# Kernel tuning notes

Measured on AMD Instinct MI355X. Metric: run time of the kernel, lower is better.

The kernel has to match this reference:

```python
import jax, jax.numpy as jnp
import numpy as np
import math

B, S, D, H = 16, 256, 1024, 16
DK = D // H
MAXLEN = 512


def _sinusoid_table(maxlen, dim):
    # rows for positions -maxlen .. maxlen-1  (2*maxlen rows)
    pos = jnp.arange(-maxlen, maxlen, dtype=jnp.float32)[:, None]
    i = jnp.arange(dim)
    angle = pos / jnp.power(10000.0, (2 * (i // 2)) / dim).astype(jnp.float32)
    return jnp.where(i % 2 == 0, jnp.sin(angle), jnp.cos(angle))


def setup_inputs() -> dict:
    key = jax.random.key(0)
    ks = jax.random.split(key, 13)
    std_qk = math.sqrt(2.0 / (D + DK))
    inp = {
        "x": jax.random.normal(ks[0], (B, S, D), jnp.float32),
        "Wq": jax.random.normal(ks[1], (D, D), jnp.float32) * std_qk,
        "bq": jnp.zeros((D,), jnp.float32),
        "Wk": jax.random.normal(ks[2], (D, D), jnp.float32) * std_qk,
        "bk": jnp.zeros((D,), jnp.float32),
        "Wv": jax.random.normal(ks[3], (D, D), jnp.float32) * std_qk,
        "bv": jnp.zeros((D,), jnp.float32),
        "Wr": jax.random.normal(ks[4], (D, D), jnp.float32) * std_qk,
        "br": jnp.zeros((D,), jnp.float32),
        "u_bias": jax.random.normal(ks[5], (H, DK), jnp.float32) * math.sqrt(2.0 / (H + DK)),
        "v_bias": jax.random.normal(ks[6], (H, DK), jnp.float32) * math.sqrt(2.0 / (H + DK)),
        "Wo": jax.random.normal(ks[7], (D, D), jnp.float32) * math.sqrt(2.0 / (D + D)),
        "bo": jnp.zeros((D,), jnp.float32),
    }
    return inp


def reference(x, Wq, bq, Wk, bk, Wv, bv, Wr, br, u_bias, v_bias, Wo, bo):
    table = _sinusoid_table(MAXLEN, D)  # (2*MAXLEN, D)
    # relative position indices: idx[s, z] = z - s, shifted by +MAXLEN
    relpos_idx = (jnp.arange(2 * S)[None, :] - jnp.arange(S)[:, None])[:, :S] + MAXLEN
    relpos_vec = table[relpos_idx]  # (S, S, D)

    q = (x @ Wq.T + bq).reshape(B, S, H, DK)
    k = (x @ Wk.T + bk).reshape(B, S, H, DK)
    v = (x @ Wv.T + bv).reshape(B, S, H, DK)

    rp_k = (relpos_vec @ Wk.T + bk).reshape(S, S, H, DK)       # shared k_proj
    kR = (x @ Wr.T + br).reshape(B, S, H, DK)                  # relpos_k_proj(keys)
    rp_R = (relpos_vec @ Wr.T + br).reshape(S, S, H, DK)       # relpos_k_proj(relpos)

    w = jnp.einsum('bshd,bzhd->bhsz', q, k)
    w = w + jnp.einsum('bshd,szhd->bhsz', q, rp_k)
    w = w + jnp.einsum('hd,bzhd->bhz', u_bias, kR)[:, :, None, :]
    w = w + jnp.einsum('hd,szhd->hsz', v_bias, rp_R)[None, :, :, :]
    w = w / math.sqrt(DK)

    causal = jnp.tril(jnp.ones((S, S), jnp.float32))[None, None, :, :]
    w = w + jnp.log(causal)  # -inf above diagonal

    attn = jax.nn.softmax(w, axis=-1)                          # (B,H,S,S)
    vw = jnp.einsum('bhsz,bzhd->bshd', attn, v).reshape(B, S, D)
    return vw @ Wo.T + bo
```

## Files before the change

### kernel.cpp

```cpp
#include <hip/hip_runtime.h>
#include <math.h>

constexpr int kB  = 16;
constexpr int kS  = 256;
constexpr int kD  = 1024;
constexpr int kH  = 16;
constexpr float kScale = 0.125f;

using bf16x8  = __attribute__((ext_vector_type(8))) short;
using floatx4 = __attribute__((ext_vector_type(4))) float;
typedef unsigned short u16;

__device__ __forceinline__ u16 f2bf(float x) {
  union { float f; unsigned u; } v; v.f = x;
  unsigned r = v.u + 0x7fffu + ((v.u >> 16) & 1u);
  return (u16)(r >> 16);
}
__device__ __forceinline__ float bf2f(u16 h) {
  union { unsigned u; float f; } v; v.u = ((unsigned)h) << 16;
  return v.f;
}

#define MFMA16(a, b, c) __builtin_amdgcn_mfma_f32_16x16x32_bf16((a), (b), (c), 0, 0, 0)
#define GLL16(gp, lp)                                                        \
  __builtin_amdgcn_global_load_lds(                                          \
      (const __attribute__((address_space(1))) unsigned int*)(gp),           \
      (__attribute__((address_space(3))) unsigned int*)(lp), 16, 0, 0)

__global__ __launch_bounds__(256) void pack_k(
    const float* __restrict__ x, const float* __restrict__ Wq,
    const float* __restrict__ Wk, const float* __restrict__ Wv,
    const float* __restrict__ Wo,
    const float* __restrict__ bq, const float* __restrict__ bk,
    const float* __restrict__ bv,
    u16* __restrict__ xA, u16* __restrict__ W3b, u16* __restrict__ Wob,
    float* __restrict__ b3) {
  size_t i = ((size_t)blockIdx.x * 256 + threadIdx.x) * 4;
  const size_t NX = (size_t)4194304, NW = (size_t)1048576;
  const size_t BEND = NX + 4 * NW + 3072;
  const float* src;
  u16* dst;
  size_t o;
  if (i < NX) {
    src = x; dst = xA; o = i;
  } else if (i < NX + 3 * NW) {
    size_t j = i - NX;
    int sel = (int)(j >> 20);
    o = j & (NW - 1);
    src = sel == 0 ? Wq : sel == 1 ? Wv : Wk;
    dst = W3b + (size_t)sel * NW;
  } else if (i < NX + 4 * NW) {
    o = i - NX - 3 * NW;
    src = Wo; dst = Wob;
  } else if (i < BEND) {
    size_t j = i - NX - 4 * NW;
    int sel = (int)(j >> 10);
    o = j & 1023;
    src = sel == 0 ? bq : sel == 1 ? bv : bk;
    *reinterpret_cast<float4*>(b3 + j) = *reinterpret_cast<const float4*>(src + o);
    return;
  } else if (i < BEND + 262144) {
    size_t j = i - BEND;
    int p = (int)(j >> 10);
    int ibase = (int)(j & 1023);
    ushort4 r;
    u16* rr = (u16*)&r;
#pragma unroll
    for (int c = 0; c < 4; ++c) {
      int idx = ibase + c;
      float ex = (float)(2 * (idx / 2)) * (1.0f / 1024.0f);
      float scale = exp2f(ex * -13.287712379549449f);
      float angle = (float)(p - 255) * scale;
      rr[c] = f2bf((idx & 1) ? cosf(angle) : sinf(angle));
    }
    *reinterpret_cast<ushort4*>(xA + NX + j) = r;
    return;
  } else {
    return;
  }
  float4 v = *reinterpret_cast<const float4*>(src + o);
  ushort4 r;
  r.x = f2bf(v.x); r.y = f2bf(v.y); r.z = f2bf(v.z); r.w = f2bf(v.w);
  *reinterpret_cast<ushort4*>(dst + o) = r;
}

__global__ __launch_bounds__(256) void uv_fold_k(
    const float* __restrict__ Wr, const float* __restrict__ br,
    const float* __restrict__ ub, const float* __restrict__ vb,
    u16* __restrict__ W3b, float* __restrict__ b3) {
  int gid = blockIdx.x * 256 + threadIdx.x;
  int j = gid >> 10, c = gid & 1023;
  int h = j & 15;
  const float* bvec = (j < 16 ? ub : vb) + h * 64;
  const float* wcol = Wr + (size_t)(h * 64) * 1024 + c;
  float a = 0.f;
#pragma unroll
  for (int d = 0; d < 64; ++d) a += bvec[d] * wcol[(size_t)d * 1024];
  W3b[(size_t)(3072 + j) * 1024 + c] = f2bf(a);
  if (gid < 128) {
    float s = 0.f;
    if (gid < 32) {
      const float* bv2 = (gid < 16 ? ub : vb) + (gid & 15) * 64;
      const float* brp = br + (gid & 15) * 64;
      for (int d = 0; d < 64; ++d) s += bv2[d] * brp[d];
    }
    b3[3072 + gid] = s;
  }
}

template <int OUT_MODE>
__global__ __launch_bounds__(256) void gemm_k(
    const u16* __restrict__ A, const u16* __restrict__ W,
    const float* __restrict__ bias, void* __restrict__ Cv,
    int M, int N, int K, float* __restrict__ utb, float* __restrict__ dtb,
    int mTiles, int nTiles) {
  const int xcd = blockIdx.x & 7;
  const int li  = blockIdx.x >> 3;
  const int r0   = (xcd * mTiles) >> 3;
  const int rcnt = (((xcd + 1) * mTiles) >> 3) - r0;
  if (li >= rcnt * nTiles) return;
  const int bm = (r0 + li % rcnt) * 128;
  const int bn = (li / rcnt) * 128;

  __shared__ u16 Alds[128 * 64];
  __shared__ u16 Blds[128 * 64];
  const int t = threadIdx.x, w = t >> 6, l = t & 63;
  const int l15 = l & 15, quad = l >> 4;
  const int wm = w >> 1, wn = w & 1;
  const int lrow8 = l >> 3;
  const int kslot = l & 7;

  floatx4 acc[4][4] = {};

  for (int k0 = 0; k0 < K; k0 += 64) {
#pragma unroll
    for (int sg = 0; sg < 4; ++sg) {
      int mrow = sg * 32 + w * 8 + lrow8;
      int gk = (kslot ^ (mrow & 7)) << 3;
      GLL16(A + (size_t)(bm + mrow) * K + k0 + gk, Alds + (sg * 32 + w * 8) * 64);
      GLL16(W + (size_t)(bn + mrow) * K + k0 + gk, Blds + (sg * 32 + w * 8) * 64);
    }
    __syncthreads();
#pragma unroll
    for (int c = 0; c < 2; ++c) {
      bf16x8 af[4], bf[4];
#pragma unroll
      for (int mi = 0; mi < 4; ++mi) {
        int am = wm * 64 + mi * 16 + l15;
        af[mi] = *(const bf16x8*)(Alds + am * 64 + (((c * 4 + quad) ^ (am & 7)) << 3));
      }
#pragma unroll
      for (int ni = 0; ni < 4; ++ni) {
        int an = wn * 64 + ni * 16 + l15;
        bf[ni] = *(const bf16x8*)(Blds + an * 64 + (((c * 4 + quad) ^ (an & 7)) << 3));
      }
#pragma unroll
      for (int mi = 0; mi < 4; ++mi)
#pragma unroll
        for (int ni = 0; ni < 4; ++ni)
          acc[mi][ni] = MFMA16(af[mi], bf[ni], acc[mi][ni]);
    }
    __syncthreads();
  }

#pragma unroll
  for (int ni = 0; ni < 4; ++ni) {
    int col = bn + wn * 64 + ni * 16 + l15;
    float bv = bias[col];
#pragma unroll
    for (int mi = 0; mi < 4; ++mi) {
      int mrow = bm + wm * 64 + mi * 16 + quad * 4;
#pragma unroll
      for (int r = 0; r < 4; ++r) {
        float v = acc[mi][ni][r] + bv;
        int row = mrow + r;
        if (OUT_MODE == 0) {
          ((float*)Cv)[(size_t)row * N + col] = v;
        }
      }
    }
  }
}

#define PHASE_MFMA(aa, bb, mh, nh)                                             \
  do {                                                                         \
    __builtin_amdgcn_s_barrier();                                              \
    asm volatile("s_waitcnt lgkmcnt(0)" ::: "memory");                         \
    __builtin_amdgcn_sched_barrier(0);                                         \
    __builtin_amdgcn_s_setprio(1);                                             \
    _Pragma("unroll") for (int kc = 0; kc < 2; ++kc)                           \
        _Pragma("unroll") for (int i = 0; i < 4; ++i)                          \
            _Pragma("unroll") for (int j = 0; j < 2; ++j)                      \
                acc[(mh) * 4 + i][(nh) * 2 + j] = MFMA16(                      \
                    aa[kc][i], bb[kc][j], acc[(mh) * 4 + i][(nh) * 2 + j]);    \
    __builtin_amdgcn_s_setprio(0);                                             \
  } while (0)

__global__ __launch_bounds__(512, 2) void gemm256_k(
    const u16* __restrict__ A, const u16* __restrict__ W,
    const float* __restrict__ bias, u16* __restrict__ Cv,
    int K, float* __restrict__ utb, float* __restrict__ dtb,
    int mTiles, int nTiles) {
  const int nwg = mTiles * nTiles;
  const int qq = nwg >> 3, rr = nwg & 7;
  const int xcd = blockIdx.x & 7;
  const int wgid = (xcd < rr ? xcd * (qq + 1) : rr * (qq + 1) + (xcd - rr) * qq)
                   + (blockIdx.x >> 3);
  const int bm = (wgid / nTiles) * 256;
  const int bn = (wgid % nTiles) * 256;

  __shared__ u16 lds[2 * 32768];

  const int t = threadIdx.x, w = t >> 6, l = t & 63;
  const int l15 = l & 15, quad = l >> 4;
  const int wm = w >> 2, wn = w & 3;

  const int NT = K >> 6;
  floatx4 acc[8][4] = {};

  auto stage = [&](int kt, int h) {
    const u16* srcm = (h < 2) ? A : W;
    const int baser = ((h < 2) ? bm : bn) + (h & 1) * 128;
    u16* dst = lds + (kt & 1) * 32768 + h * 8192 + w * 512;
    const int k0 = kt << 6;
#pragma unroll
    for (int j = 0; j < 2; ++j) {
      int sub = w * 8 + (l >> 3) + j * 64;
      int gk = ((l & 7) ^ (sub & 7)) << 3;
      GLL16(srcm + (size_t)(baser + sub) * K + k0 + gk, dst + j * 4096);
    }
  };

  stage(0, 2); stage(0, 3); stage(0, 0); stage(0, 1);
  stage(1, 2); stage(1, 3); stage(1, 0);
  asm volatile("s_waitcnt vmcnt(6)" ::: "memory");
  __builtin_amdgcn_s_barrier();

  for (int kt = 0; kt < NT; ++kt) {
    const u16* LA = lds + (kt & 1) * 32768;
    const u16* LB = LA + 16384;
    bf16x8 a0[2][4], a1[2][4], b0[2][2], b1[2][2];

#pragma unroll
    for (int i = 0; i < 4; ++i) {
      int am = wm * 128 + i * 16 + l15;
      const u16* p = LA + am * 64;
      a0[0][i] = *(const bf16x8*)(p + ((quad ^ (am & 7)) << 3));
      a0[1][i] = *(const bf16x8*)(p + (((4 + quad) ^ (am & 7)) << 3));
    }
#pragma unroll
    for (int j = 0; j < 2; ++j) {
      int an = wn * 64 + j * 16 + l15;
      const u16* p = LB + an * 64;
      b0[0][j] = *(const bf16x8*)(p + ((quad ^ (an & 7)) << 3));
      b0[1][j] = *(const bf16x8*)(p + (((4 + quad) ^ (an & 7)) << 3));
    }
    if (kt + 1 < NT) stage(kt + 1, 1);
    PHASE_MFMA(a0, b0, 0, 0);
    __builtin_amdgcn_s_barrier();

#pragma unroll
    for (int j = 0; j < 2; ++j) {
      int an = wn * 64 + (2 + j) * 16 + l15;
      const u16* p = LB + an * 64;
      b1[0][j] = *(const bf16x8*)(p + ((quad ^ (an & 7)) << 3));
      b1[1][j] = *(const bf16x8*)(p + (((4 + quad) ^ (an & 7)) << 3));
    }
    PHASE_MFMA(a0, b1, 0, 1);
    __builtin_amdgcn_s_barrier();

#pragma unroll
    for (int i = 0; i < 4; ++i) {
      int am = wm * 128 + (4 + i) * 16 + l15;
      const u16* p = LA + am * 64;
      a1[0][i] = *(const bf16x8*)(p + ((quad ^ (am & 7)) << 3));
      a1[1][i] = *(const bf16x8*)(p + (((4 + quad) ^ (am & 7)) << 3));
    }
    if (kt + 2 < NT) stage(kt + 2, 2);
    PHASE_MFMA(a1, b0, 1, 0);
    __builtin_amdgcn_s_barrier();

    if (kt + 2 < NT) { stage(kt + 2, 3); stage(kt + 2, 0); }
    PHASE_MFMA(a1, b1, 1, 1);
    if (kt + 2 < NT) {
      asm volatile("s_waitcnt vmcnt(6)" ::: "memory");
    } else {
      asm volatile("s_waitcnt vmcnt(0)" ::: "memory");
    }
    __builtin_amdgcn_s_barrier();
  }

#pragma unroll
  for (int ni = 0; ni < 4; ++ni) {
    int col = bn + wn * 64 + ni * 16 + l15;
    float bv = bias[col];
#pragma unroll
    for (int mi = 0; mi < 8; ++mi) {
      int mrow = bm + wm * 128 + mi * 16 + quad * 4;
#pragma unroll
      for (int r = 0; r < 4; ++r) {
        float v = acc[mi][ni][r] + bv;
        int row = mrow + r;
        if (col < 3072) {
          int matsel = col >> 10;
          int hh = (col >> 6) & 15, dd = col & 63;
          if (row < 4096) {
            int bb = row >> 8, ss = row & 255;
            Cv[(size_t)matsel * 4194304 +
               ((size_t)(((bb << 4) + hh) << 8) + ss) * 64 + dd] = f2bf(v);
          } else if (matsel == 2) {
            int pp = row - 4096;
            Cv[(size_t)3 * 4194304 +
               ((size_t)((hh << 8) + pp)) * 64 + dd] = f2bf(v);
          }
        } else if (col < 3088) {
          if (row < 4096)
            utb[((row >> 8) * 16 + (col - 3072)) * 256 + (row & 255)] = v;
        } else if (col < 3104) {
          if (row >= 4096)
            dtb[(col - 3088) * 256 + (row - 4096)] = v;
        }
      }
    }
  }
}

__global__ __launch_bounds__(512, 2) void attn_k(
    const u16* __restrict__ Qh, const u16* __restrict__ Kh,
    const u16* __restrict__ Vh, const u16* __restrict__ RPKh,
    const float* __restrict__ ut, const float* __restrict__ dt,
    u16* __restrict__ vw) {
  __shared__ u16 Klds[256 * 64];
  __shared__ u16 Vt[64][280];
  __shared__ float Sc[32][257];
  __shared__ float Sc2[32][257];
  __shared__ float Ut[256], Dt[256], Rinv[32];

  const int bh = blockIdx.x;
  const int h = bh & 15;
  const int b = bh >> 4;
  const size_t bh256 = (size_t)bh << 8;

  const int t = threadIdx.x, w = t >> 6, l = t & 63;
  const int l15 = l & 15, quad = l >> 4;

  {
    const int lrow8 = l >> 3, kslot = l & 7;
#pragma unroll
    for (int i = 0; i < 4; ++i) {
      int row = w * 32 + i * 8 + lrow8;
      int gk = (kslot ^ (row & 7)) << 3;
      GLL16(Kh + (bh256 + row) * 64 + gk, Klds + (w * 32 + i * 8) * 64);
    }
  }
  {
    int z = t & 255, dh = t >> 8;
    const u16* gp = Vh + (bh256 + z) * 64 + dh * 32;
    ushort4 vv[8];
#pragma unroll
    for (int i = 0; i < 8; ++i) vv[i] = *(const ushort4*)(gp + i * 4);
#pragma unroll
    for (int i = 0; i < 8; ++i) {
      Vt[dh * 32 + i * 4 + 0][z] = vv[i].x;
      Vt[dh * 32 + i * 4 + 1][z] = vv[i].y;
      Vt[dh * 32 + i * 4 + 2][z] = vv[i].z;
      Vt[dh * 32 + i * 4 + 3][z] = vv[i].w;
    }
  }
  if (t < 256) Ut[t] = ut[bh256 + t];
  else         Dt[t - 256] = dt[((size_t)h << 8) + (t - 256)];
  __syncthreads();

  for (int st = 0; st < 8; ++st) {
    const int s0 = st * 32;

    bf16x8 qa[2][2];
#pragma unroll
    for (int rt = 0; rt < 2; ++rt) {
      const u16* qp = Qh + (bh256 + s0 + rt * 16 + l15) * 64 + quad * 8;
      qa[rt][0] = *(const bf16x8*)qp;
      qa[rt][1] = *(const bf16x8*)(qp + 32);
    }

    {
      int cnt = 0;
#pragma unroll
      for (int rt = 0; rt < 2; ++rt) {
        const int rB = s0 + rt * 16;
        const int nzt = 2 * st + rt + 1;
        for (int zt = 0; zt < nzt; ++zt, ++cnt) {
          if ((cnt & 7) != w) continue;
          const int zr = (zt << 4) + l15;
          const u16* krow = Klds + zr * 64;
          bf16x8 kb0 = *(const bf16x8*)(krow + ((quad ^ (zr & 7)) << 3));
          bf16x8 kb1 = *(const bf16x8*)(krow + (((quad + 4) ^ (zr & 7)) << 3));
          floatx4 acc = {};
          acc = MFMA16(qa[rt][0], kb0, acc);
          acc = MFMA16(qa[rt][1], kb1, acc);
          float u = Ut[zr];
#pragma unroll
          for (int r = 0; r < 4; ++r)
            Sc[rt * 16 + quad * 4 + r][zr] = acc[r] + u;
        }
        for (int j = 0; j < nzt; ++j, ++cnt) {
          if ((cnt & 7) != w) continue;
          const int pr = 240 - rB + (j << 4) + l15;
          const u16* rp = RPKh + ((size_t)(h << 8) + pr) * 64 + quad * 8;
          bf16x8 rb0 = *(const bf16x8*)rp;
          bf16x8 rb1 = *(const bf16x8*)(rp + 32);
          floatx4 acc = {};
          acc = MFMA16(qa[rt][0], rb0, acc);
          acc = MFMA16(qa[rt][1], rb1, acc);
          float dv = Dt[pr];
#pragma unroll
          for (int r = 0; r < 4; ++r)
            Sc2[rt * 16 + quad * 4 + r][pr] = acc[r] + dv;
        }
      }
    }
    __syncthreads();

    {
      const int row = w * 4 + (l >> 4);
      const int c16 = l & 15;
      const int s = s0 + row;
      const int zfill = 32 * (st + 1);
      float m = -1e30f;
      for (int z = c16; z <= s; z += 16)
        m = fmaxf(m, Sc[row][z] + Sc2[row][z - s + 255]);
      m = fmaxf(m, __shfl_xor(m, 1));
      m = fmaxf(m, __shfl_xor(m, 2));
      m = fmaxf(m, __shfl_xor(m, 4));
      m = fmaxf(m, __shfl_xor(m, 8));
      m *= kScale;
      float sum = 0.f;
      for (int z = c16; z < zfill; z += 16) {
        float e = 0.f;
        if (z <= s) {
          e = __expf((Sc[row][z] + Sc2[row][z - s + 255]) * kScale - m);
          sum += e;
        }
        Sc[row][z] = e;
      }
      sum += __shfl_xor(sum, 1);
      sum += __shfl_xor(sum, 2);
      sum += __shfl_xor(sum, 4);
      sum += __shfl_xor(sum, 8);
      if (c16 == 0) Rinv[row] = 1.f / sum;
    }
    __syncthreads();

    {
      const int strip = w >> 2, nt = w & 3;
      const int sB = s0 + strip * 16;
      floatx4 oacc = {};
      for (int kc = 0; kc <= st; ++kc) {
        const float* prow = &Sc[strip * 16 + l15][kc * 32 + quad * 8];
        bf16x8 pa;
        pa[0] = (short)f2bf(prow[0]); pa[1] = (short)f2bf(prow[1]);
        pa[2] = (short)f2bf(prow[2]); pa[3] = (short)f2bf(prow[3]);
        pa[4] = (short)f2bf(prow[4]); pa[5] = (short)f2bf(prow[5]);
        pa[6] = (short)f2bf(prow[6]); pa[7] = (short)f2bf(prow[7]);
        const u16* vp = &Vt[nt * 16 + l15][kc * 32 + quad * 8];
        bf16x8 vbf = *(const bf16x8*)vp;
        oacc = MFMA16(pa, vbf, oacc);
      }
#pragma unroll
      for (int r = 0; r < 4; ++r) {
        float ivr = Rinv[strip * 16 + quad * 4 + r];
        int srow = sB + quad * 4 + r;
        vw[(size_t)(b * 256 + srow) * 1024 + h * 64 + nt * 16 + l15] =
            f2bf(oacc[r] * ivr);
      }
    }
    __syncthreads();
  }
}

extern "C" void kernel_launch(void* const* d_in, const int* in_sizes, int n_in,
                              void* d_out, int out_size, void* d_ws, size_t ws_size,
                              hipStream_t stream) {
  const float* x  = (const float*)d_in[0];
  const float* Wq = (const float*)d_in[1];
  const float* bq = (const float*)d_in[2];
  const float* Wk = (const float*)d_in[3];
  const float* bk = (const float*)d_in[4];
  const float* Wv = (const float*)d_in[5];
  const float* bv = (const float*)d_in[6];
  const float* Wr = (const float*)d_in[7];
  const float* br = (const float*)d_in[8];
  const float* ub = (const float*)d_in[9];
  const float* vb = (const float*)d_in[10];
  const float* Wo = (const float*)d_in[11];
  const float* bo = (const float*)d_in[12];
  float* out = (float*)d_out;

  char* base = (char*)d_ws;
  size_t off = 0;
  auto alloc = [&](size_t bytes) {
    void* p = base + off;
    off += (bytes + 255) & ~(size_t)255;
    return p;
  };

  const size_t MAT = (size_t)4194304;
  u16*   xA    = (u16*)alloc((size_t)4352 * 1024 * 2);
  u16*   W3b   = (u16*)alloc((size_t)3328 * 1024 * 2);
  u16*   Wob   = (u16*)alloc((size_t)1024 * 1024 * 2);
  float* b3    = (float*)alloc((size_t)3328 * 4);
  u16*   Ph    = (u16*)alloc((3 * MAT + 262144) * 2);
  float* utb   = (float*)alloc((size_t)65536 * 4);
  float* dtb   = (float*)alloc((size_t)4096 * 4);
  u16*   vwb   = (u16*)alloc((size_t)4096 * 1024 * 2);

  u16* Qh   = Ph;
  u16* Vh   = Ph + MAT;
  u16* Kh   = Ph + 2 * MAT;
  u16* RPKh = Ph + 3 * MAT;

  pack_k<<<dim3(8451), dim3(256), 0, stream>>>(x, Wq, Wk, Wv, Wo, bq, bk, bv,
                                               xA, W3b, Wob, b3);
  uv_fold_k<<<dim3(128), dim3(256), 0, stream>>>(Wr, br, ub, vb, W3b, b3);

  gemm256_k<<<dim3(221), dim3(512), 0, stream>>>(xA, W3b, b3, Ph,
                                                 1024, utb, dtb, 17, 13);

  attn_k<<<dim3(256), dim3(512), 0, stream>>>(Qh, Kh, Vh, RPKh, utb, dtb, vwb);

  gemm_k<0><<<dim3(256), dim3(256), 0, stream>>>(vwb, Wob, bo, out,
                                                 4096, 1024, 1024, nullptr, nullptr,
                                                 32, 8);
}
```

Before: 223.7 us.

## Prefetch LDS fragments across GEMM phases and stage epilogue through LDS for vector stores

The big projection GEMM now issues LDS reads for the next phase's fragments before the current phase's MFMAs, using partial lgkmcnt waits. It also prefetches the next k-tile's A/B fragments during the last MFMA phase, so LDS latency is hidden behind matrix math. The epilogue writes accumulators into swizzled LDS in two halves, then reads them back as float4 to emit coalesced 8-byte bf16 stores instead of scattered 2-byte stores. This adds register pressure from fragments kept live across iterations, plus extra barriers in the epilogue.

```diff
diff --git a/kernel.cpp b/kernel.cpp
--- a/kernel.cpp
+++ b/kernel.cpp
@@ -182,10 +182,10 @@
   }
 }
 
-#define PHASE_MFMA(aa, bb, mh, nh)                                             \
+#define PHASE_MFMA(aa, bb, mh, nh, LG)                                         \
   do {                                                                         \
     __builtin_amdgcn_s_barrier();                                              \
-    asm volatile("s_waitcnt lgkmcnt(0)" ::: "memory");                         \
+    asm volatile("s_waitcnt lgkmcnt(" #LG ")" ::: "memory");                   \
     __builtin_amdgcn_sched_barrier(0);                                         \
     __builtin_amdgcn_s_setprio(1);                                             \
     _Pragma("unroll") for (int kc = 0; kc < 2; ++kc)                           \
@@ -202,9 +202,9 @@
     int K, float* __restrict__ utb, float* __restrict__ dtb,
     int mTiles, int nTiles) {
   const int nwg = mTiles * nTiles;
-  const int qq = nwg >> 3, rr = nwg & 7;
+  const int qq = nwg >> 3, rr8 = nwg & 7;
   const int xcd = blockIdx.x & 7;
-  const int wgid = (xcd < rr ? xcd * (qq + 1) : rr * (qq + 1) + (xcd - rr) * qq)
+  const int wgid = (xcd < rr8 ? xcd * (qq + 1) : rr8 * (qq + 1) + (xcd - rr8) * qq)
                    + (blockIdx.x >> 3);
   const int bm = (wgid / nTiles) * 256;
   const int bn = (wgid % nTiles) * 256;
@@ -231,94 +231,134 @@
     }
   };
 
+  bf16x8 a0[2][4], a1[2][4], b0[2][2], b1[2][2];
+
+  auto readA = [&](bf16x8 (&aa)[2][4], const u16* LA, int hh) {
+#pragma unroll
+    for (int i = 0; i < 4; ++i) {
+      int am = wm * 128 + hh * 64 + i * 16 + l15;
+      const u16* p = LA + am * 64;
+      aa[0][i] = *(const bf16x8*)(p + ((quad ^ (am & 7)) << 3));
+      aa[1][i] = *(const bf16x8*)(p + (((4 + quad) ^ (am & 7)) << 3));
+    }
+  };
+  auto readB = [&](bf16x8 (&bb)[2][2], const u16* LB, int hh) {
+#pragma unroll
+    for (int j = 0; j < 2; ++j) {
+      int an = wn * 64 + hh * 32 + j * 16 + l15;
+      const u16* p = LB + an * 64;
+      bb[0][j] = *(const bf16x8*)(p + ((quad ^ (an & 7)) << 3));
+      bb[1][j] = *(const bf16x8*)(p + (((4 + quad) ^ (an & 7)) << 3));
+    }
+  };
+
   stage(0, 2); stage(0, 3); stage(0, 0); stage(0, 1);
   stage(1, 2); stage(1, 3); stage(1, 0);
   asm volatile("s_waitcnt vmcnt(6)" ::: "memory");
   __builtin_amdgcn_s_barrier();
+  readA(a0, lds, 0);
+  readB(b0, lds + 16384, 0);
 
   for (int kt = 0; kt < NT; ++kt) {
     const u16* LA = lds + (kt & 1) * 32768;
     const u16* LB = LA + 16384;
-    bf16x8 a0[2][4], a1[2][4], b0[2][2], b1[2][2];
-
-#pragma unroll
-    for (int i = 0; i < 4; ++i) {
-      int am = wm * 128 + i * 16 + l15;
-      const u16* p = LA + am * 64;
-      a0[0][i] = *(const bf16x8*)(p + ((quad ^ (am & 7)) << 3));
-      a0[1][i] = *(const bf16x8*)(p + (((4 + quad) ^ (am & 7)) << 3));
-    }
-#pragma unroll
-    for (int j = 0; j < 2; ++j) {
-      int an = wn * 64 + j * 16 + l15;
-      const u16* p = LB + an * 64;
-      b0[0][j] = *(const bf16x8*)(p + ((quad ^ (an & 7)) << 3));
-      b0[1][j] = *(const bf16x8*)(p + (((4 + quad) ^ (an & 7)) << 3));
-    }
+
+    readB(b1, LB, 1);
     if (kt + 1 < NT) stage(kt + 1, 1);
-    PHASE_MFMA(a0, b0, 0, 0);
+    PHASE_MFMA(a0, b0, 0, 0, 4);
     __builtin_amdgcn_s_barrier();
 
-#pragma unroll
-    for (int j = 0; j < 2; ++j) {
-      int an = wn * 64 + (2 + j) * 16 + l15;
-      const u16* p = LB + an * 64;
-      b1[0][j] = *(const bf16x8*)(p + ((quad ^ (an & 7)) << 3));
-      b1[1][j] = *(const bf16x8*)(p + (((4 + quad) ^ (an & 7)) << 3));
-    }
-    PHASE_MFMA(a0, b1, 0, 1);
+    readA(a1, LA, 1);
+    PHASE_MFMA(a0, b1, 0, 1, 8);
     __builtin_amdgcn_s_barrier();
 
-#pragma unroll
-    for (int i = 0; i < 4; ++i) {
-      int am = wm * 128 + (4 + i) * 16 + l15;
-      const u16* p = LA + am * 64;
-      a1[0][i] = *(const bf16x8*)(p + ((quad ^ (am & 7)) << 3));
-      a1[1][i] = *(const bf16x8*)(p + (((4 + quad) ^ (am & 7)) << 3));
-    }
     if (kt + 2 < NT) stage(kt + 2, 2);
-    PHASE_MFMA(a1, b0, 1, 0);
+    PHASE_MFMA(a1, b0, 1, 0, 0);
     __builtin_amdgcn_s_barrier();
 
-    if (kt + 2 < NT) { stage(kt + 2, 3); stage(kt + 2, 0); }
-    PHASE_MFMA(a1, b1, 1, 1);
     if (kt + 2 < NT) {
+      stage(kt + 2, 3); stage(kt + 2, 0);
       asm volatile("s_waitcnt vmcnt(6)" ::: "memory");
     } else {
       asm volatile("s_waitcnt vmcnt(0)" ::: "memory");
     }
     __builtin_amdgcn_s_barrier();
-  }
-
-#pragma unroll
-  for (int ni = 0; ni < 4; ++ni) {
-    int col = bn + wn * 64 + ni * 16 + l15;
-    float bv = bias[col];
-#pragma unroll
-    for (int mi = 0; mi < 8; ++mi) {
-      int mrow = bm + wm * 128 + mi * 16 + quad * 4;
-#pragma unroll
-      for (int r = 0; r < 4; ++r) {
-        float v = acc[mi][ni][r] + bv;
-        int row = mrow + r;
-        if (col < 3072) {
-          int matsel = col >> 10;
-          int hh = (col >> 6) & 15, dd = col & 63;
-          if (row < 4096) {
-            int bb = row >> 8, ss = row & 255;
-            Cv[(size_t)matsel * 4194304 +
-               ((size_t)(((bb << 4) + hh) << 8) + ss) * 64 + dd] = f2bf(v);
+    asm volatile("s_waitcnt lgkmcnt(0)" ::: "memory");
+    __builtin_amdgcn_sched_barrier(0);
+    if (kt + 1 < NT) {
+      const u16* LAn = lds + ((kt + 1) & 1) * 32768;
+      readA(a0, LAn, 0);
+      readB(b0, LAn + 16384, 0);
+    }
+    __builtin_amdgcn_s_setprio(1);
+#pragma unroll
+    for (int kc = 0; kc < 2; ++kc)
+#pragma unroll
+      for (int i = 0; i < 4; ++i)
+#pragma unroll
+        for (int j = 0; j < 2; ++j)
+          acc[4 + i][2 + j] = MFMA16(a1[kc][i], b1[kc][j], acc[4 + i][2 + j]);
+    __builtin_amdgcn_s_setprio(0);
+    __builtin_amdgcn_s_barrier();
+  }
+
+  float* fl = (float*)lds;
+#pragma unroll 1
+  for (int half = 0; half < 2; ++half) {
+    __syncthreads();
+    if (wm == half) {
+#pragma unroll
+      for (int ni = 0; ni < 4; ++ni) {
+        float bv = bias[bn + wn * 64 + ni * 16 + l15];
+#pragma unroll
+        for (int mi = 0; mi < 8; ++mi) {
+#pragma unroll
+          for (int r = 0; r < 4; ++r) {
+            int lr = mi * 16 + quad * 4 + r;
+            int c  = wn * 64 + ni * 16 + l15;
+            int key = ((r ^ quad) & 3) << 4;
+            fl[lr * 256 + (c ^ key)] = acc[mi][ni][r] + bv;
+          }
+        }
+      }
+    }
+    __syncthreads();
+#pragma unroll 1
+    for (int cc = 0; cc < 4; ++cc) {
+      int col0 = bn + cc * 64;
+#pragma unroll
+      for (int rr = 0; rr < 4; ++rr) {
+        int lr = w * 16 + rr * 4 + quad;
+        int key = ((rr ^ quad) & 3) << 4;
+        float4 v = *(const float4*)&fl[lr * 256 + ((cc * 64 + (l15 << 2)) ^ key)];
+        int grow = bm + half * 128 + lr;
+        if (col0 < 3072) {
+          ushort4 hv;
+          hv.x = f2bf(v.x); hv.y = f2bf(v.y); hv.z = f2bf(v.z); hv.w = f2bf(v.w);
+          int matsel = col0 >> 10;
+          int hh2 = (col0 >> 6) & 15;
+          if (grow < 4096) {
+            int bb = grow >> 8, ss = grow & 255;
+            *(ushort4*)(Cv + (size_t)matsel * 4194304 +
+                        ((size_t)(((bb << 4) + hh2) << 8) + ss) * 64 + (l15 << 2)) = hv;
           } else if (matsel == 2) {
-            int pp = row - 4096;
-            Cv[(size_t)3 * 4194304 +
-               ((size_t)((hh << 8) + pp)) * 64 + dd] = f2bf(v);
+            int pp = grow - 4096;
+            *(ushort4*)(Cv + (size_t)3 * 4194304 +
+                        ((size_t)((hh2 << 8) + pp)) * 64 + (l15 << 2)) = hv;
           }
-        } else if (col < 3088) {
-          if (row < 4096)
-            utb[((row >> 8) * 16 + (col - 3072)) * 256 + (row & 255)] = v;
-        } else if (col < 3104) {
-          if (row >= 4096)
-            dtb[(col - 3088) * 256 + (row - 4096)] = v;
+        } else if (col0 < 3104) {
+#pragma unroll
+          for (int e = 0; e < 4; ++e) {
+            int col = col0 + (l15 << 2) + e;
+            float vv = e == 0 ? v.x : e == 1 ? v.y : e == 2 ? v.z : v.w;
+            if (col < 3088) {
+              if (grow < 4096)
+                utb[((grow >> 8) * 16 + (col - 3072)) * 256 + (grow & 255)] = vv;
+            } else if (col < 3104) {
+              if (grow >= 4096)
+                dtb[(col - 3088) * 256 + (grow - 4096)] = vv;
+            }
+          }
         }
       }
     }
```

Result: no change. 221.1 us (-1.2%).
